# Optimization experiments

Measured on AMD Instinct MI355X. Metric: run time of the kernel, lower is better.

## Reference

```python
import jax, jax.numpy as jnp
import numpy as np

N_NODES = 100000
N_EDGES = 1000000
D_IN = 64
D_OUT = 64


def setup_inputs() -> dict:
    key = jax.random.key(0)
    k1, k2, k3, k4, k5 = jax.random.split(key, 5)
    x = jax.random.normal(k1, (N_NODES, D_IN), dtype=jnp.float32)
    W = jax.random.normal(k2, (D_OUT, D_IN), dtype=jnp.float32) / np.sqrt(D_IN)
    edge_weights = jax.random.uniform(k3, (N_EDGES,), dtype=jnp.float32)
    source = jax.random.randint(k4, (N_EDGES,), 0, N_NODES, dtype=jnp.int64 if jax.config.read('jax_enable_x64') else jnp.int32)
    target = jax.random.randint(k5, (N_EDGES,), 0, N_NODES, dtype=jnp.int64 if jax.config.read('jax_enable_x64') else jnp.int32)
    return {"x": x, "W": W, "edge_weights": edge_weights,
            "source": source, "target": target, "num_nodes": N_NODES}


def reference(x, W, edge_weights, source, target, num_nodes):
    # Linear (no bias): h = x @ W^T, shape (num_nodes, out)
    h = jnp.einsum('nd,od->no', x, W)
    # Gather messages per edge, scale by edge weights
    msg = h[source] * edge_weights[:, None]  # (num_edges, out)
    # Scatter-add by target node (sum aggregation)
    delta = jax.ops.segment_sum(msg, target, num_segments=num_nodes)
    return delta
```

## Files before the change

### kernel.cpp

```cpp
#include <hip/hip_runtime.h>


#define D     64
#define BKT   64
#define BSH   6
#define NBMAX 2048
#define CAP   1024
#define CAPB  1024

__global__ __launch_bounds__(256) void gcn_scatter_kernel(
    const float* __restrict__ x, const float* __restrict__ ew,
    const int* __restrict__ src, const int* __restrict__ tgt,
    float* __restrict__ s, int n_edges)
{
    int lane = threadIdx.x & 63;
    int e = blockIdx.x * 4 + (threadIdx.x >> 6);
    if (e >= n_edges) return;
    int sn = src[e];
    int tn = tgt[e];
    float w = ew[e];
    float v = x[(size_t)sn * D + lane] * w;
    atomicAdd(&s[(size_t)tn * D + lane], v);
}

__global__ __launch_bounds__(256) void gcn_gemm_kernel(
    const float* __restrict__ s, const float* __restrict__ W,
    float* __restrict__ out, int n_nodes)
{
    __shared__ float4 xs[64 * 17];
    const int tid  = threadIdx.x;
    const int lane = tid & 63;
    const int wid  = __builtin_amdgcn_readfirstlane(tid >> 6);
    const int row0 = blockIdx.x * 64;

    const float4* s4 = reinterpret_cast<const float4*>(s);
#pragma unroll
    for (int k = 0; k < 4; ++k) {
        int f  = tid + k * 256;
        int r  = f >> 4;
        int c4 = f & 15;
        float4 v = make_float4(0.f, 0.f, 0.f, 0.f);
        if (row0 + r < n_nodes)
            v = s4[(size_t)(row0 + r) * 16 + c4];
        xs[r * 17 + c4] = v;
    }
    __syncthreads();

    float acc[16];
#pragma unroll
    for (int j = 0; j < 16; ++j) acc[j] = 0.f;

    const int o0 = wid * 16;
    const float4* W4 = reinterpret_cast<const float4*>(W);
#pragma unroll
    for (int d4 = 0; d4 < 16; ++d4) {
        float4 xv = xs[lane * 17 + d4];
#pragma unroll
        for (int j = 0; j < 16; ++j) {
            float4 wv = W4[(size_t)(o0 + j) * 16 + d4];
            acc[j] += xv.x * wv.x + xv.y * wv.y + xv.z * wv.z + xv.w * wv.w;
        }
    }

    const int row = row0 + lane;
    if (row < n_nodes) {
        float4* out4 = reinterpret_cast<float4*>(out);
#pragma unroll
        for (int j4 = 0; j4 < 4; ++j4) {
            float4 v = make_float4(acc[j4 * 4 + 0], acc[j4 * 4 + 1],
                                   acc[j4 * 4 + 2], acc[j4 * 4 + 3]);
            out4[(size_t)row * 16 + wid * 4 + j4] = v;
        }
    }
}

__device__ __forceinline__ unsigned f2bf(float f) {
    unsigned u = __float_as_uint(f);
    return (u + 0x7FFFu + ((u >> 16) & 1u)) >> 16;
}

__global__ __launch_bounds__(256) void convert_init_kernel(
    const float* __restrict__ x, uint2* __restrict__ xb, int n4,
    int* __restrict__ bbeg, int* __restrict__ bcur, int nb)
{
    const int g = blockIdx.x * 256 + threadIdx.x;
    if (g < nb) { bbeg[g] = g * CAPB; bcur[g] = g * CAPB; }
    const float4* x4 = reinterpret_cast<const float4*>(x);
    for (int i = g; i < n4; i += gridDim.x * 256) {
        float4 v = x4[i];
        uint2 o;
        o.x = f2bf(v.x) | (f2bf(v.y) << 16);
        o.y = f2bf(v.z) | (f2bf(v.w) << 16);
        xb[i] = o;
    }
}

__global__ __launch_bounds__(256) void convert_hist_kernel(
    const float* __restrict__ x, uint2* __restrict__ xb, int n4,
    const int* __restrict__ tgt, int* __restrict__ bcnt,
    int n_edges, int nb, int epb)
{
    __shared__ int h[NBMAX];
    const int tid = threadIdx.x;
    for (int i = tid; i < nb; i += 256) h[i] = 0;

    const float4* x4 = reinterpret_cast<const float4*>(x);
    for (int i = blockIdx.x * 256 + tid; i < n4; i += gridDim.x * 256) {
        float4 v = x4[i];
        uint2 o;
        o.x = f2bf(v.x) | (f2bf(v.y) << 16);
        o.y = f2bf(v.z) | (f2bf(v.w) << 16);
        xb[i] = o;
    }
    __syncthreads();

    const int e0 = blockIdx.x * epb;
    const int e1 = min(e0 + epb, n_edges);
    for (int e = e0 + tid; e < e1; e += 256)
        atomicAdd(&h[tgt[e] >> BSH], 1);
    __syncthreads();
    for (int b = tid; b < nb; b += 256) {
        int c = h[b];
        if (c) atomicAdd(&bcnt[b], c);
    }
}

__global__ __launch_bounds__(1024) void bucket_scan_kernel(
    const int* __restrict__ bcnt, int* __restrict__ bstarts,
    int* __restrict__ bcur, int nb, int n_edges)
{
    __shared__ int lds[1024];
    const int tid = threadIdx.x;
    const int i0 = 2 * tid, i1 = 2 * tid + 1;
    int v0 = (i0 < nb) ? bcnt[i0] : 0;
    int v1 = (i1 < nb) ? bcnt[i1] : 0;
    int tsum = v0 + v1;
    lds[tid] = tsum;
    __syncthreads();
    for (int off = 1; off < 1024; off <<= 1) {
        int a = (tid >= off) ? lds[tid - off] : 0;
        __syncthreads();
        lds[tid] += a;
        __syncthreads();
    }
    int pre = lds[tid] - tsum;
    if (i0 < nb) { bstarts[i0] = pre;      bcur[i0] = pre; }
    if (i1 < nb) { bstarts[i1] = pre + v0; bcur[i1] = pre + v0; }
    if (tid == 0) bstarts[nb] = n_edges;
}

__global__ __launch_bounds__(256) void bucket_scatter_kernel(
    const int* __restrict__ src, const int* __restrict__ tgt,
    const float* __restrict__ ew, int* __restrict__ bcur,
    int2* __restrict__ pairs, int n_edges, int nb, int epb)
{
    __shared__ int h[NBMAX];
    __shared__ int base[NBMAX];
    const int tid = threadIdx.x;
    for (int i = tid; i < nb; i += 256) h[i] = 0;
    __syncthreads();
    const int e0 = blockIdx.x * epb;
    const int e1 = min(e0 + epb, n_edges);

    for (int e = e0 + tid; e < e1; e += 256)
        atomicAdd(&h[tgt[e] >> BSH], 1);
    __syncthreads();

    for (int b = tid; b < nb; b += 256) {
        int c = h[b];
        base[b] = c ? atomicAdd(&bcur[b], c) : 0;
        h[b] = 0;
    }
    __syncthreads();

    for (int e = e0 + tid; e < e1; e += 256) {
        int t = tgt[e];
        int b = t >> BSH;
        int r = atomicAdd(&h[b], 1);
        pairs[base[b] + r] =
            make_int2(((t & (BKT - 1)) << 24) | src[e], __float_as_int(ew[e]));
    }
}

__global__ __launch_bounds__(512, 8) void bucket_sort_reduce_gemm_kernel(
    const uint2* __restrict__ xb, const float* __restrict__ W,
    const int* __restrict__ bbeg, const int* __restrict__ bend,
    const int2* __restrict__ pairs,
    float* __restrict__ out, int n_nodes, int nb)
{
    __shared__ float Wl[64 * 66];
    __shared__ int2  ep[CAP];
    __shared__ int   segIncl[BKT];
    __shared__ int   rankc[BKT];
    __shared__ float accRow[8][64];

    const int tid  = threadIdx.x;
    const int lane = tid & 63;
    const int wv   = tid >> 6;
    const int q4   = lane >> 4;
    const int m    = lane & 15;

    for (int i = tid; i < 64 * 64; i += 512)
        Wl[(i >> 6) * 66 + (i & 63)] = W[i];

    const int b   = blockIdx.x;
    const int beg = bbeg[b];
    const int end = bend[b];

    float4 acc[8];
#pragma unroll
    for (int s = 0; s < 8; ++s) acc[s] = make_float4(0.f, 0.f, 0.f, 0.f);

    for (int cbeg = beg; cbeg < end; cbeg += CAP) {
        const int ccnt = min(CAP, end - cbeg);

        int2 pr0 = make_int2(0, 0), pr1 = make_int2(0, 0);
        if (tid < ccnt)       pr0 = pairs[cbeg + tid];
        if (tid + 512 < ccnt) pr1 = pairs[cbeg + tid + 512];

        if (tid < BKT) segIncl[tid] = 0;
        __syncthreads();

        if (tid < ccnt)       atomicAdd(&segIncl[((unsigned)pr0.x) >> 24], 1);
        if (tid + 512 < ccnt) atomicAdd(&segIncl[((unsigned)pr1.x) >> 24], 1);
        __syncthreads();

        if (wv == 0) {
            int c0 = segIncl[lane];
            int v = c0;
#pragma unroll
            for (int off = 1; off < 64; off <<= 1) {
                int n = __shfl_up(v, off);
                if (lane >= off) v += n;
            }
            segIncl[lane] = v;
            rankc[lane]   = v - c0;
        }
        __syncthreads();

        if (tid < ccnt) {
            int pos = atomicAdd(&rankc[((unsigned)pr0.x) >> 24], 1);
            ep[pos] = pr0;
        }
        if (tid + 512 < ccnt) {
            int pos = atomicAdd(&rankc[((unsigned)pr1.x) >> 24], 1);
            ep[pos] = pr1;
        }
        __syncthreads();

#pragma unroll
        for (int s = 0; s < 8; ++s) {
            const int tl = s * 8 + wv;
            const int s0 = __builtin_amdgcn_readfirstlane(tl ? segIncl[tl - 1] : 0);
            const int s1 = __builtin_amdgcn_readfirstlane(segIncl[tl]);
            float4 a = acc[s];
            for (int e = s0; e < s1; e += 8) {
                const int ea = e + q4;
                const int eb = e + 4 + q4;
                int2 p0 = ep[min(ea, s1 - 1)];
                int2 p1 = ep[min(eb, s1 - 1)];
                float w0 = (ea < s1) ? __int_as_float(p0.y) : 0.f;
                float w1 = (eb < s1) ? __int_as_float(p1.y) : 0.f;
                uint2 r0 = xb[(size_t)(p0.x & 0xFFFFFF) * 16 + m];
                uint2 r1 = xb[(size_t)(p1.x & 0xFFFFFF) * 16 + m];
                a.x += w0 * __uint_as_float(r0.x << 16);
                a.y += w0 * __uint_as_float(r0.x & 0xFFFF0000u);
                a.z += w0 * __uint_as_float(r0.y << 16);
                a.w += w0 * __uint_as_float(r0.y & 0xFFFF0000u);
                a.x += w1 * __uint_as_float(r1.x << 16);
                a.y += w1 * __uint_as_float(r1.x & 0xFFFF0000u);
                a.z += w1 * __uint_as_float(r1.y << 16);
                a.w += w1 * __uint_as_float(r1.y & 0xFFFF0000u);
            }
            acc[s] = a;
        }
        __syncthreads();
    }

    const int node0 = b * BKT;
#pragma unroll
    for (int s = 0; s < 8; ++s) {
        const int node = node0 + s * 8 + wv;
        if (node < n_nodes) {
            float4 a = acc[s];
            a.x += __shfl_xor(a.x, 16); a.y += __shfl_xor(a.y, 16);
            a.z += __shfl_xor(a.z, 16); a.w += __shfl_xor(a.w, 16);
            a.x += __shfl_xor(a.x, 32); a.y += __shfl_xor(a.y, 32);
            a.z += __shfl_xor(a.z, 32); a.w += __shfl_xor(a.w, 32);
            if (lane < 16)
                *reinterpret_cast<float4*>(&accRow[wv][m * 4]) = a;
            asm volatile("s_waitcnt lgkmcnt(0)" ::: "memory");

            float o = 0.f;
            const float2* a2 = reinterpret_cast<const float2*>(&accRow[wv][0]);
            const float2* w2 = reinterpret_cast<const float2*>(&Wl[lane * 66]);
#pragma unroll
            for (int d2 = 0; d2 < 32; ++d2) {
                float2 aq = a2[d2];
                float2 wq = w2[d2];
                o += aq.x * wq.x + aq.y * wq.y;
            }
            out[(size_t)node * D + lane] = o;
            asm volatile("s_waitcnt lgkmcnt(0)" ::: "memory");
        }
    }
}

extern "C" void kernel_launch(void* const* d_in, const int* in_sizes, int n_in,
                              void* d_out, int out_size, void* d_ws, size_t ws_size,
                              hipStream_t stream)
{
    const float* x   = (const float*)d_in[0];
    const float* W   = (const float*)d_in[1];
    const float* ew  = (const float*)d_in[2];
    const int*   src = (const int*)d_in[3];
    const int*   tgt = (const int*)d_in[4];

    const int n_nodes = in_sizes[0] / D;
    const int n_edges = in_sizes[2];
    const int nb = (n_nodes + BKT - 1) / BKT;
    const int cblocks = 256;
    const int epbC = (n_edges + cblocks - 1) / cblocks;

    {
        int*   bcur  = (int*)d_ws;
        int*   bbeg  = bcur + nb;
        size_t ints  = 2 * (size_t)nb;
        ints = (ints + 1) & ~(size_t)1;
        int2*  pairs = (int2*)((int*)d_ws + ints);
        uint2* xb    = (uint2*)(pairs + (size_t)nb * CAPB);
        const size_t need = ints * 4 + (size_t)nb * CAPB * 8 +
                            (size_t)n_nodes * 128;

        if (nb <= NBMAX && n_nodes <= (1 << 24) && ws_size >= need) {
            convert_init_kernel<<<256, 256, 0, stream>>>(
                x, xb, n_nodes * 16, bbeg, bcur, nb);
            bucket_scatter_kernel<<<cblocks, 256, 0, stream>>>(
                src, tgt, ew, bcur, pairs, n_edges, nb, epbC);
            bucket_sort_reduce_gemm_kernel<<<nb, 512, 0, stream>>>(
                xb, W, bbeg, bcur, pairs, (float*)d_out, n_nodes, nb);
            return;
        }
    }

    {
        int*   bcnt    = (int*)d_ws;
        int*   bstarts = bcnt + NBMAX;
        int*   bcur    = bstarts + NBMAX + 1;
        size_t ints    = 3 * (size_t)NBMAX + 1;
        ints = (ints + 1) & ~(size_t)1;
        int2*  pairs   = (int2*)((int*)d_ws + ints);
        uint2* xb      = (uint2*)(pairs + n_edges);
        const size_t need = ints * 4 + (size_t)n_edges * 8 +
                            (size_t)n_nodes * 128;

        if (nb <= NBMAX && n_nodes <= (1 << 24) && ws_size >= need) {
            hipMemsetAsync(bcnt, 0, (size_t)nb * sizeof(int), stream);
            const int ablocks = 256;
            const int epbA = (n_edges + ablocks - 1) / ablocks;
            convert_hist_kernel<<<ablocks, 256, 0, stream>>>(
                x, xb, n_nodes * 16, tgt, bcnt, n_edges, nb, epbA);
            bucket_scan_kernel<<<1, 1024, 0, stream>>>(bcnt, bstarts, bcur,
                                                       nb, n_edges);
            bucket_scatter_kernel<<<cblocks, 256, 0, stream>>>(
                src, tgt, ew, bcur, pairs, n_edges, nb, epbC);
            bucket_sort_reduce_gemm_kernel<<<nb, 512, 0, stream>>>(
                xb, W, bstarts, bstarts + 1, pairs, (float*)d_out, n_nodes, nb);
            return;
        }
    }

    float* s = (float*)d_ws;
    hipMemsetAsync(s, 0, (size_t)n_nodes * D * sizeof(float), stream);
    gcn_scatter_kernel<<<(n_edges + 3) / 4, 256, 0, stream>>>(x, ew, src, tgt, s, n_edges);
    gcn_gemm_kernel<<<(n_nodes + 63) / 64, 256, 0, stream>>>(s, W, (float*)d_out, n_nodes);
}
```

Measured before the change: 119.1 us.

## Sort bucket edges by source-node class and accumulate via LDS atomics

Within each destination bucket, edges are now grouped into 16 classes by source-node range rather than by target row. This is meant to improve locality of the gathered bf16 x rows across concurrently running blocks. Per-row register accumulation with shuffle reductions is replaced by float atomicAdd into a shared 64x65 accumulator, which the final GEMM reads directly. This adds LDS atomic contention and more shared memory (launch bounds drop from 8 to 6 blocks), in exchange for better-balanced work across waves.

```diff
diff --git a/kernel.cpp b/kernel.cpp
--- a/kernel.cpp
+++ b/kernel.cpp
@@ -7,6 +7,7 @@
 #define NBMAX 2048
 #define CAP   1024
 #define CAPB  1024
+#define NCLS  16
 
 __global__ __launch_bounds__(256) void gcn_scatter_kernel(
     const float* __restrict__ x, const float* __restrict__ ew,
@@ -182,97 +183,91 @@
     }
 }
 
-__global__ __launch_bounds__(512, 8) void bucket_sort_reduce_gemm_kernel(
+__global__ __launch_bounds__(512, 6) void bucket_class_reduce_gemm_kernel(
     const uint2* __restrict__ xb, const float* __restrict__ W,
     const int* __restrict__ bbeg, const int* __restrict__ bend,
     const int2* __restrict__ pairs,
-    float* __restrict__ out, int n_nodes, int nb)
+    float* __restrict__ out, int n_nodes, int nb, int csh)
 {
     __shared__ float Wl[64 * 66];
+    __shared__ float accS[64 * 65];
     __shared__ int2  ep[CAP];
-    __shared__ int   segIncl[BKT];
-    __shared__ int   rankc[BKT];
-    __shared__ float accRow[8][64];
+    __shared__ int   clsIncl[NCLS];
+    __shared__ int   clsRank[NCLS];
 
     const int tid  = threadIdx.x;
     const int lane = tid & 63;
     const int wv   = tid >> 6;
-    const int q4   = lane >> 4;
-    const int m    = lane & 15;
+    const int m    = tid & 15;
+    const int qg   = tid >> 4;
 
     for (int i = tid; i < 64 * 64; i += 512)
         Wl[(i >> 6) * 66 + (i & 63)] = W[i];
+    for (int i = tid; i < 64 * 65; i += 512) accS[i] = 0.f;
 
     const int b   = blockIdx.x;
     const int beg = bbeg[b];
     const int end = bend[b];
-
-    float4 acc[8];
-#pragma unroll
-    for (int s = 0; s < 8; ++s) acc[s] = make_float4(0.f, 0.f, 0.f, 0.f);
+    __syncthreads();
 
     for (int cbeg = beg; cbeg < end; cbeg += CAP) {
         const int ccnt = min(CAP, end - cbeg);
 
         int2 pr0 = make_int2(0, 0), pr1 = make_int2(0, 0);
-        if (tid < ccnt)       pr0 = pairs[cbeg + tid];
-        if (tid + 512 < ccnt) pr1 = pairs[cbeg + tid + 512];
-
-        if (tid < BKT) segIncl[tid] = 0;
-        __syncthreads();
-
-        if (tid < ccnt)       atomicAdd(&segIncl[((unsigned)pr0.x) >> 24], 1);
-        if (tid + 512 < ccnt) atomicAdd(&segIncl[((unsigned)pr1.x) >> 24], 1);
-        __syncthreads();
-
-        if (wv == 0) {
-            int c0 = segIncl[lane];
+        int  cls0 = 0, cls1 = 0;
+        if (tid < ccnt) {
+            pr0 = pairs[cbeg + tid];
+            cls0 = min((pr0.x & 0xFFFFFF) >> csh, NCLS - 1);
+        }
+        if (tid + 512 < ccnt) {
+            pr1 = pairs[cbeg + tid + 512];
+            cls1 = min((pr1.x & 0xFFFFFF) >> csh, NCLS - 1);
+        }
+
+        if (tid < NCLS) clsIncl[tid] = 0;
+        __syncthreads();
+        if (tid < ccnt)       atomicAdd(&clsIncl[cls0], 1);
+        if (tid + 512 < ccnt) atomicAdd(&clsIncl[cls1], 1);
+        __syncthreads();
+
+        if (wv == 0 && lane < NCLS) {
+            int c0 = clsIncl[lane];
             int v = c0;
 #pragma unroll
-            for (int off = 1; off < 64; off <<= 1) {
-                int n = __shfl_up(v, off);
-                if (lane >= off) v += n;
+            for (int off = 1; off < NCLS; off <<= 1) {
+                int nv = __shfl_up(v, off);
+                if (lane >= off) v += nv;
             }
-            segIncl[lane] = v;
-            rankc[lane]   = v - c0;
+            clsIncl[lane] = v;
+            clsRank[lane] = v - c0;
         }
         __syncthreads();
 
         if (tid < ccnt) {
-            int pos = atomicAdd(&rankc[((unsigned)pr0.x) >> 24], 1);
-            ep[pos] = pr0;
+            int p = atomicAdd(&clsRank[cls0], 1);
+            ep[p] = pr0;
         }
         if (tid + 512 < ccnt) {
-            int pos = atomicAdd(&rankc[((unsigned)pr1.x) >> 24], 1);
-            ep[pos] = pr1;
-        }
-        __syncthreads();
-
-#pragma unroll
-        for (int s = 0; s < 8; ++s) {
-            const int tl = s * 8 + wv;
-            const int s0 = __builtin_amdgcn_readfirstlane(tl ? segIncl[tl - 1] : 0);
-            const int s1 = __builtin_amdgcn_readfirstlane(segIncl[tl]);
-            float4 a = acc[s];
-            for (int e = s0; e < s1; e += 8) {
-                const int ea = e + q4;
-                const int eb = e + 4 + q4;
-                int2 p0 = ep[min(ea, s1 - 1)];
-                int2 p1 = ep[min(eb, s1 - 1)];
-                float w0 = (ea < s1) ? __int_as_float(p0.y) : 0.f;
-                float w1 = (eb < s1) ? __int_as_float(p1.y) : 0.f;
-                uint2 r0 = xb[(size_t)(p0.x & 0xFFFFFF) * 16 + m];
-                uint2 r1 = xb[(size_t)(p1.x & 0xFFFFFF) * 16 + m];
-                a.x += w0 * __uint_as_float(r0.x << 16);
-                a.y += w0 * __uint_as_float(r0.x & 0xFFFF0000u);
-                a.z += w0 * __uint_as_float(r0.y << 16);
-                a.w += w0 * __uint_as_float(r0.y & 0xFFFF0000u);
-                a.x += w1 * __uint_as_float(r1.x << 16);
-                a.y += w1 * __uint_as_float(r1.x & 0xFFFF0000u);
-                a.z += w1 * __uint_as_float(r1.y << 16);
-                a.w += w1 * __uint_as_float(r1.y & 0xFFFF0000u);
+            int p = atomicAdd(&clsRank[cls1], 1);
+            ep[p] = pr1;
+        }
+        __syncthreads();
+
+        for (int c = 0; c < NCLS; ++c) {
+            const int ce0 = __builtin_amdgcn_readfirstlane(c ? clsIncl[c - 1] : 0);
+            const int ce1 = __builtin_amdgcn_readfirstlane(clsIncl[c]);
+            for (int e = ce0 + qg; e < ce1; e += 32) {
+                int2 p = ep[e];
+                const int   tl = ((unsigned)p.x) >> 24;
+                const int   sn = p.x & 0xFFFFFF;
+                const float w  = __int_as_float(p.y);
+                uint2 r = xb[(size_t)sn * 16 + m];
+                float* ab = &accS[tl * 65 + m * 4];
+                atomicAdd(&ab[0], w * __uint_as_float(r.x << 16));
+                atomicAdd(&ab[1], w * __uint_as_float(r.x & 0xFFFF0000u));
+                atomicAdd(&ab[2], w * __uint_as_float(r.y << 16));
+                atomicAdd(&ab[3], w * __uint_as_float(r.y & 0xFFFF0000u));
             }
-            acc[s] = a;
         }
         __syncthreads();
     }
@@ -280,28 +275,16 @@
     const int node0 = b * BKT;
 #pragma unroll
     for (int s = 0; s < 8; ++s) {
-        const int node = node0 + s * 8 + wv;
+        const int tl = s * 8 + wv;
+        const int node = node0 + tl;
         if (node < n_nodes) {
-            float4 a = acc[s];
-            a.x += __shfl_xor(a.x, 16); a.y += __shfl_xor(a.y, 16);
-            a.z += __shfl_xor(a.z, 16); a.w += __shfl_xor(a.w, 16);
-            a.x += __shfl_xor(a.x, 32); a.y += __shfl_xor(a.y, 32);
-            a.z += __shfl_xor(a.z, 32); a.w += __shfl_xor(a.w, 32);
-            if (lane < 16)
-                *reinterpret_cast<float4*>(&accRow[wv][m * 4]) = a;
-            asm volatile("s_waitcnt lgkmcnt(0)" ::: "memory");
-
+            const float* ar = &accS[tl * 65];
+            const float* wr = &Wl[lane * 66];
             float o = 0.f;
-            const float2* a2 = reinterpret_cast<const float2*>(&accRow[wv][0]);
-            const float2* w2 = reinterpret_cast<const float2*>(&Wl[lane * 66]);
-#pragma unroll
-            for (int d2 = 0; d2 < 32; ++d2) {
-                float2 aq = a2[d2];
-                float2 wq = w2[d2];
-                o += aq.x * wq.x + aq.y * wq.y;
-            }
+#pragma unroll
+            for (int d = 0; d < 64; ++d)
+                o += ar[d] * wr[d];
             out[(size_t)node * D + lane] = o;
-            asm volatile("s_waitcnt lgkmcnt(0)" ::: "memory");
         }
     }
 }
@@ -321,6 +304,9 @@
     const int nb = (n_nodes + BKT - 1) / BKT;
     const int cblocks = 256;
     const int epbC = (n_edges + cblocks - 1) / cblocks;
+
+    int csh = 0;
+    while (((n_nodes - 1) >> csh) > (NCLS - 1)) ++csh;
 
     {
         int*   bcur  = (int*)d_ws;
@@ -337,8 +323,8 @@
                 x, xb, n_nodes * 16, bbeg, bcur, nb);
             bucket_scatter_kernel<<<cblocks, 256, 0, stream>>>(
                 src, tgt, ew, bcur, pairs, n_edges, nb, epbC);
-            bucket_sort_reduce_gemm_kernel<<<nb, 512, 0, stream>>>(
-                xb, W, bbeg, bcur, pairs, (float*)d_out, n_nodes, nb);
+            bucket_class_reduce_gemm_kernel<<<nb, 512, 0, stream>>>(
+                xb, W, bbeg, bcur, pairs, (float*)d_out, n_nodes, nb, csh);
             return;
         }
     }
@@ -364,8 +350,8 @@
                                                        nb, n_edges);
             bucket_scatter_kernel<<<cblocks, 256, 0, stream>>>(
                 src, tgt, ew, bcur, pairs, n_edges, nb, epbC);
-            bucket_sort_reduce_gemm_kernel<<<nb, 512, 0, stream>>>(
-                xb, W, bstarts, bstarts + 1, pairs, (float*)d_out, n_nodes, nb);
+            bucket_class_reduce_gemm_kernel<<<nb, 512, 0, stream>>>(
+                xb, W, bstarts, bstarts + 1, pairs, (float*)d_out, n_nodes, nb, csh);
             return;
         }
     }
```

Result: slower. 467.3 us (+292.3%).
